# Optimization experiments

Measured on AMD Instinct MI355X. Metric: run time of the kernel, lower is better.

The kernel has to match this reference:

```python
import jax, jax.numpy as jnp
import numpy as np
from jax import lax

T = 64      # timesteps == number of stacked LSTM layers (per source)
B = 128     # lstm_batchsize (hardcoded)
H = 64      # BasicLSTMCell(64)


def _cell(x_in, c, h, W, b):
    # TF BasicLSTMCell, forget_bias=0.0, gate order: i, j, f, o
    z = jnp.concatenate([x_in, h], axis=-1) @ W + b          # [B, 4H]
    i, j, f, o = jnp.split(z, 4, axis=-1)
    c2 = c * jax.nn.sigmoid(f) + jax.nn.sigmoid(i) * jnp.tanh(j)
    h2 = jnp.tanh(c2) * jax.nn.sigmoid(o)
    return c2, h2


def setup_inputs() -> dict:
    key = jax.random.key(0)
    ks = jax.random.split(key, 8)
    s = 0.1
    x = jax.random.normal(ks[0], (B, T, 1), dtype=jnp.float32)
    labels = jax.random.normal(ks[1], (B, T, 1), dtype=jnp.float32)
    # layer 0: input dim 1; layers 1..T-1: input dim H
    W0 = jax.random.normal(ks[2], (1 + H, 4 * H), dtype=jnp.float32) * s
    b0 = jnp.zeros((4 * H,), dtype=jnp.float32)
    Wl = jax.random.normal(ks[3], (T - 1, H + H, 4 * H), dtype=jnp.float32) * s
    bl = jnp.zeros((T - 1, 4 * H), dtype=jnp.float32)
    # time_distributed fully_connected(1, relu): separate weights per timestep
    Wd = jax.random.normal(ks[4], (T, H, 1), dtype=jnp.float32) * s
    bd = jnp.zeros((T, 1), dtype=jnp.float32)
    return {"x": x, "labels": labels, "W0": W0, "b0": b0,
            "Wl": Wl, "bl": bl, "Wd": Wd, "bd": bd}


def reference(x, labels, W0, b0, Wl, bl, Wd, bd):
    def step(carry, x_t):
        cs, hs = carry                      # each [T, B, H]
        c0, h0 = _cell(x_t, cs[0], hs[0], W0, b0)

        def layer_step(h_in, lp):
            c, h_prev, W, b = lp
            c2, h2 = _cell(h_in, c, h_prev, W, b)
            return h2, (c2, h2)

        h_top, (cs_r, hs_r) = lax.scan(layer_step, h0, (cs[1:], hs[1:], Wl, bl))
        new_cs = jnp.concatenate([c0[None], cs_r], axis=0)
        new_hs = jnp.concatenate([h0[None], hs_r], axis=0)
        return (new_cs, new_hs), h_top

    init = (jnp.zeros((T, B, H), x.dtype), jnp.zeros((T, B, H), x.dtype))
    xs = jnp.transpose(x, (1, 0, 2))        # [T, B, 1]
    _, outs = lax.scan(step, init, xs)      # outs: [T, B, H]
    outs = jnp.transpose(outs, (1, 0, 2))   # [B, T, H]

    # per-timestep dense + relu
    pred = jax.nn.relu(jnp.einsum('bth,tho->bto', outs, Wd) + bd[None])  # [B, T, 1]
    loss = jnp.mean(jnp.square(labels - pred))
    return pred, loss
```

## Files before the change

### kernel.cpp

```cpp
#include <hip/hip_runtime.h>
#include <hip/hip_bf16.h>
#include <hip/hip_fp8.h>

#define TT 64
#define LL 64
#define BB 128
#define HH 64
#define NP 32
#define SL 8
#define RR 16

typedef short v8s __attribute__((ext_vector_type(8)));
typedef float v4f __attribute__((ext_vector_type(4)));


__device__ __forceinline__ float sigm(float z)   {
    return __builtin_amdgcn_rcpf(1.f + __expf(-z));
}
__device__ __forceinline__ float tanh_f(float z) {
    return fmaf(-2.f, __builtin_amdgcn_rcpf(1.f + __expf(2.f * z)), 1.f);
}
__device__ __forceinline__ unsigned long long gload64(const unsigned long long* p) {
    return __hip_atomic_load(p, __ATOMIC_RELAXED, __HIP_MEMORY_SCOPE_AGENT);
}
__device__ __forceinline__ void gstore64(unsigned long long* p, unsigned long long v) {
    __hip_atomic_store(p, v, __ATOMIC_RELAXED, __HIP_MEMORY_SCOPE_AGENT);
}
__device__ __forceinline__ int fload(const int* p) {
    return __hip_atomic_load(p, __ATOMIC_RELAXED, __HIP_MEMORY_SCOPE_AGENT);
}
__device__ __forceinline__ void fstore(int* p, int v) {
    __hip_atomic_store(p, v, __ATOMIC_RELAXED, __HIP_MEMORY_SCOPE_AGENT);
}
__device__ __forceinline__ unsigned short f2bf(float f) {
    unsigned u = __float_as_uint(f);
    return (unsigned short)((u + 0x8000u) >> 16);
}

__global__ __launch_bounds__(512, 2) void lstm_pipeline(
    const float* __restrict__ x,
    const float* __restrict__ W0,
    const float* __restrict__ b0,
    const float* __restrict__ Wl,
    const float* __restrict__ bl,
    int* __restrict__ prog,
    unsigned long long* __restrict__ hglob,
    float* __restrict__ htop)
{
    const int p   = blockIdx.x >> 3;
    const int s   = blockIdx.x & 7;
    const int tid = threadIdx.x;
    const int wv  = tid >> 6;
    const int la  = wv >> 2;
    const int w   = wv & 3;
    const int ln  = tid & 63;
    const int lr  = ln & 15;
    const int qd  = ln >> 4;
    const int l   = 2 * p + la;

    __shared__ unsigned short hA[2][RR * 72];
    __shared__ unsigned short hB[2][RR * 72];
    __shared__ float xbuf[RR * 65];

    if (blockIdx.x == 0 && tid < 2) fstore(&prog[300 + tid], 0);

    for (int i = tid; i < RR * 72; i += 512) {
        hA[0][i] = 0; hA[1][i] = 0; hB[0][i] = 0; hB[1][i] = 0;
    }
    if (p == 0) {
        for (int i = tid; i < RR * 64; i += 512)
            xbuf[(i >> 6) * 65 + (i & 63)] =
                x[(size_t)(s * RR + (i >> 6)) * TT + (i & 63)];
    }

    v8s bfr[16];
#pragma unroll
    for (int f = 0; f < 16; ++f) {
        const int ga = f >> 2, kf = f & 3;
        const int gc = ga * 64 + w * 16 + lr;
        v8s tmp;
#pragma unroll
        for (int j = 0; j < 8; ++j) {
            const int k = kf * 32 + qd * 8 + j;
            float v;
            if (l > 0)       v = Wl[((size_t)(l - 1) * 128 + k) * 256 + gc];
            else if (k == 0) v = W0[gc];
            else if (k < 64) v = 0.f;
            else             v = W0[(size_t)(k - 63) * 256 + gc];
            tmp[j] = (short)f2bf(v);
        }
        bfr[f] = tmp;
    }

    const float* bs = l ? (bl + (l - 1) * 256) : b0;
    float bias[4];
#pragma unroll
    for (int ga = 0; ga < 4; ++ga) bias[ga] = bs[ga * 64 + w * 16 + lr];

    float cst[4];
#pragma unroll
    for (int i = 0; i < 4; ++i) cst[i] = 0.f;

    __syncthreads();

    for (int t = 0; t < TT; ++t) {
        const int cur = t & 1;

        if (la == 0) {
            unsigned int belowW[4];
            if (p > 0) {
                const unsigned long long* rp =
                    hglob + ((((size_t)(t & 15) * NP + (p - 1)) * SL + s) * RR + lr) * 16;
                for (;;) {
                    unsigned long long v0 = gload64(rp + qd * 2);
                    unsigned long long v1 = gload64(rp + qd * 2 + 1);
                    unsigned long long v2 = gload64(rp + 8 + qd * 2);
                    unsigned long long v3 = gload64(rp + 8 + qd * 2 + 1);
                    unsigned int ok =
                        (unsigned int)((unsigned int)(v0 >> 32) == (unsigned int)t) &
                        (unsigned int)((unsigned int)(v1 >> 32) == (unsigned int)t) &
                        (unsigned int)((unsigned int)(v2 >> 32) == (unsigned int)t) &
                        (unsigned int)((unsigned int)(v3 >> 32) == (unsigned int)t);
                    if (ok) {
                        belowW[0] = (unsigned int)v0; belowW[1] = (unsigned int)v1;
                        belowW[2] = (unsigned int)v2; belowW[3] = (unsigned int)v3;
                        break;
                    }
                }
                if (tid == 0) fstore(&prog[s * NP + p], t + 1);
            }

            v4f acc[4];
#pragma unroll
            for (int i = 0; i < 4; ++i) acc[i] = (v4f){0.f, 0.f, 0.f, 0.f};

            const int row = lr * 72;
            v8s a2 = *(const v8s*)&hA[cur ^ 1][row + qd * 8];
            v8s a3 = *(const v8s*)&hA[cur ^ 1][row + 32 + qd * 8];
            v8s a0, a1;
            if (p > 0) {
#pragma unroll
                for (int wi = 0; wi < 2; ++wi)
#pragma unroll
                    for (int bi = 0; bi < 4; ++bi) {
                        __hip_fp8_e4m3 f8;
                        f8.__x = (belowW[wi] >> (8 * bi)) & 0xff;
                        a0[wi * 4 + bi] = (short)f2bf((float)f8);
                        f8.__x = (belowW[2 + wi] >> (8 * bi)) & 0xff;
                        a1[wi * 4 + bi] = (short)f2bf((float)f8);
                    }
            } else {
                a0 = (v8s){0, 0, 0, 0, 0, 0, 0, 0};
                a1 = (v8s){0, 0, 0, 0, 0, 0, 0, 0};
                if (qd == 0) a0[0] = (short)f2bf(xbuf[lr * 65 + t]);
            }
#pragma unroll
            for (int ga = 0; ga < 4; ++ga) {
                v4f c = acc[ga];
                c = __builtin_amdgcn_mfma_f32_16x16x32_bf16(a2, bfr[ga * 4 + 2], c, 0, 0, 0);
                c = __builtin_amdgcn_mfma_f32_16x16x32_bf16(a3, bfr[ga * 4 + 3], c, 0, 0, 0);
                c = __builtin_amdgcn_mfma_f32_16x16x32_bf16(a0, bfr[ga * 4 + 0], c, 0, 0, 0);
                c = __builtin_amdgcn_mfma_f32_16x16x32_bf16(a1, bfr[ga * 4 + 1], c, 0, 0, 0);
                acc[ga] = c;
            }
#pragma unroll
            for (int r = 0; r < 4; ++r) {
                float zi = acc[0][r] + bias[0];
                float zj = acc[1][r] + bias[1];
                float zf = acc[2][r] + bias[2];
                float zo = acc[3][r] + bias[3];
                float c2 = cst[r] * sigm(zf) + sigm(zi) * tanh_f(zj);
                cst[r] = c2;
                float h2 = tanh_f(c2) * sigm(zo);
                hA[cur][(qd * 4 + r) * 72 + w * 16 + lr] = f2bf(h2);
            }
        }

        __syncthreads();

        if (la == 1) {
            int gate = 0;
            if (p < NP - 1 && t >= 15)
                gate = fload(&prog[s * NP + (p + 1)]);

            v4f acc[4];
#pragma unroll
            for (int i = 0; i < 4; ++i) acc[i] = (v4f){0.f, 0.f, 0.f, 0.f};

            const int row = lr * 72;
            v8s a2 = *(const v8s*)&hB[cur ^ 1][row + qd * 8];
            v8s a3 = *(const v8s*)&hB[cur ^ 1][row + 32 + qd * 8];
            v8s a0 = *(const v8s*)&hA[cur][row + qd * 8];
            v8s a1 = *(const v8s*)&hA[cur][row + 32 + qd * 8];
#pragma unroll
            for (int ga = 0; ga < 4; ++ga) {
                v4f c = acc[ga];
                c = __builtin_amdgcn_mfma_f32_16x16x32_bf16(a2, bfr[ga * 4 + 2], c, 0, 0, 0);
                c = __builtin_amdgcn_mfma_f32_16x16x32_bf16(a3, bfr[ga * 4 + 3], c, 0, 0, 0);
                c = __builtin_amdgcn_mfma_f32_16x16x32_bf16(a0, bfr[ga * 4 + 0], c, 0, 0, 0);
                c = __builtin_amdgcn_mfma_f32_16x16x32_bf16(a1, bfr[ga * 4 + 1], c, 0, 0, 0);
                acc[ga] = c;
            }
            if (p < NP - 1 && t >= 15 && gate < t - 14)
                while (fload(&prog[s * NP + (p + 1)]) < t - 14) {}

            unsigned long long* dst =
                hglob + ((((size_t)(t & 15) * NP + p) * SL + s) * RR) * 16;
#pragma unroll
            for (int r = 0; r < 4; ++r) {
                float zi = acc[0][r] + bias[0];
                float zj = acc[1][r] + bias[1];
                float zf = acc[2][r] + bias[2];
                float zo = acc[3][r] + bias[3];
                float c2 = cst[r] * sigm(zf) + sigm(zi) * tanh_f(zj);
                cst[r] = c2;
                float h2 = tanh_f(c2) * sigm(zo);
                const int b = qd * 4 + r;
                const int u = w * 16 + lr;
                hB[cur][b * 72 + u] = f2bf(h2);
                if (p < NP - 1) {
                    __hip_fp8_e4m3 f8(h2);
                    unsigned int pk = ((unsigned int)f8.__x) << (8 * (lr & 3));
                    pk |= __shfl_xor(pk, 1);
                    pk |= __shfl_xor(pk, 2);
                    if ((lr & 3) == 0)
                        gstore64(dst + (size_t)b * 16 + w * 4 + (lr >> 2),
                                 (unsigned long long)pk |
                                 ((unsigned long long)(unsigned int)t << 32));
                } else {
                    htop[((size_t)t * HH + u) * BB + s * RR + b] = h2;
                }
            }
        }
    }
}

__global__ __launch_bounds__(128, 1) void epilogue(
    const float* __restrict__ htop, const float* __restrict__ Wd,
    const float* __restrict__ bd, const float* __restrict__ labels,
    float* __restrict__ out, int* __restrict__ prog)
{
    int t = blockIdx.x, b = threadIdx.x;
    float s = 0.f;
#pragma unroll 4
    for (int h = 0; h < HH; ++h)
        s = fmaf(htop[(size_t)t * HH * BB + h * BB + b], Wd[t * HH + h], s);
    s += bd[t];
    s = fmaxf(s, 0.f);
    out[b * TT + t] = s;
    float d = labels[b * TT + t] - s;
    float e = d * d;
#pragma unroll
    for (int off = 32; off > 0; off >>= 1) e += __shfl_down(e, off, 64);
    __shared__ float ws2[2];
    if ((b & 63) == 0) ws2[b >> 6] = e;
    __syncthreads();
    if (b == 0) {
        float* loss = (float*)&prog[300];
        atomicAdd(loss, ws2[0] + ws2[1]);
        __builtin_amdgcn_s_waitcnt(0);
        int done = __hip_atomic_fetch_add(&prog[301], 1, __ATOMIC_ACQ_REL,
                                          __HIP_MEMORY_SCOPE_AGENT);
        if (done == 63) {
            float tot = __hip_atomic_load(loss, __ATOMIC_RELAXED,
                                          __HIP_MEMORY_SCOPE_AGENT);
            out[BB * TT] = tot * (1.f / (BB * TT));
        }
    }
}

extern "C" void kernel_launch(void* const* d_in, const int* in_sizes, int n_in,
                              void* d_out, int out_size, void* d_ws, size_t ws_size,
                              hipStream_t stream) {
    const float* x      = (const float*)d_in[0];
    const float* labels = (const float*)d_in[1];
    const float* W0     = (const float*)d_in[2];
    const float* b0     = (const float*)d_in[3];
    const float* Wl     = (const float*)d_in[4];
    const float* bl     = (const float*)d_in[5];
    const float* Wd     = (const float*)d_in[6];
    const float* bd     = (const float*)d_in[7];
    float* out = (float*)d_out;

    char* base = (char*)d_ws;
    int*                prog  = (int*)base;
    unsigned long long* hglob = (unsigned long long*)(base + 16384);
    float*              htop  = (float*)(base + 16384 + 8388608);

    lstm_pipeline<<<NP * SL, 512, 0, stream>>>(x, W0, b0, Wl, bl, prog, hglob, htop);
    epilogue<<<64, 128, 0, stream>>>(htop, Wd, bd, labels, out, prog);
}
```

Baseline: 577.4 us.

## Pack four layers per block with in-block wavefront skew over timesteps

Each block now handles four consecutive layers instead of two. Pairs of waves own one layer and split the 64 hidden units in half, and the layers run as a diagonal wavefront inside the block, with layer k lagging k steps and one barrier per superstep. This halves the number of inter-block global handoffs (fp8 hglob and flag polling) and the grid size, cutting cross-block sync latency along the layer chain. In exchange each wave holds twice the weight fragments (32 v8s), adds GG-1 pipeline fill steps, and puts more serial work in each block.

```diff
diff --git a/kernel.cpp b/kernel.cpp
--- a/kernel.cpp
+++ b/kernel.cpp
@@ -6,9 +6,11 @@
 #define LL 64
 #define BB 128
 #define HH 64
-#define NP 32
+#define GG 4
+#define NG 16
 #define SL 8
 #define RR 16
+#define SB (TT + GG - 1)
 
 typedef short v8s __attribute__((ext_vector_type(8)));
 typedef float v4f __attribute__((ext_vector_type(4)));
@@ -47,70 +49,81 @@
     unsigned long long* __restrict__ hglob,
     float* __restrict__ htop)
 {
-    const int p   = blockIdx.x >> 3;
+    const int g   = blockIdx.x >> 3;
     const int s   = blockIdx.x & 7;
     const int tid = threadIdx.x;
     const int wv  = tid >> 6;
-    const int la  = wv >> 2;
-    const int w   = wv & 3;
+    const int k   = wv >> 1;
+    const int nh  = wv & 1;
     const int ln  = tid & 63;
     const int lr  = ln & 15;
     const int qd  = ln >> 4;
-    const int l   = 2 * p + la;
-
-    __shared__ unsigned short hA[2][RR * 72];
-    __shared__ unsigned short hB[2][RR * 72];
+    const int l   = GG * g + k;
+
+    __shared__ unsigned short hL[GG][2][RR * 72];
     __shared__ float xbuf[RR * 65];
 
     if (blockIdx.x == 0 && tid < 2) fstore(&prog[300 + tid], 0);
 
-    for (int i = tid; i < RR * 72; i += 512) {
-        hA[0][i] = 0; hA[1][i] = 0; hB[0][i] = 0; hB[1][i] = 0;
-    }
-    if (p == 0) {
+    for (int i = tid; i < GG * 2 * RR * 72; i += 512)
+        ((unsigned short*)hL)[i] = 0;
+    if (g == 0) {
         for (int i = tid; i < RR * 64; i += 512)
             xbuf[(i >> 6) * 65 + (i & 63)] =
                 x[(size_t)(s * RR + (i >> 6)) * TT + (i & 63)];
     }
 
-    v8s bfr[16];
-#pragma unroll
-    for (int f = 0; f < 16; ++f) {
-        const int ga = f >> 2, kf = f & 3;
-        const int gc = ga * 64 + w * 16 + lr;
+    v8s bfr[32];
+#pragma unroll
+    for (int f = 0; f < 32; ++f) {
+        const int kf = f & 3, tn = f >> 2;
+        const int ga = tn & 3, ut = tn >> 2;
+        const int gc = ga * 64 + nh * 32 + ut * 16 + lr;
         v8s tmp;
 #pragma unroll
         for (int j = 0; j < 8; ++j) {
-            const int k = kf * 32 + qd * 8 + j;
+            const int kk = kf * 32 + qd * 8 + j;
             float v;
-            if (l > 0)       v = Wl[((size_t)(l - 1) * 128 + k) * 256 + gc];
-            else if (k == 0) v = W0[gc];
-            else if (k < 64) v = 0.f;
-            else             v = W0[(size_t)(k - 63) * 256 + gc];
+            if (l > 0)        v = Wl[((size_t)(l - 1) * 128 + kk) * 256 + gc];
+            else if (kk == 0) v = W0[gc];
+            else if (kk < 64) v = 0.f;
+            else              v = W0[(size_t)(kk - 63) * 256 + gc];
             tmp[j] = (short)f2bf(v);
         }
         bfr[f] = tmp;
     }
 
     const float* bs = l ? (bl + (l - 1) * 256) : b0;
-    float bias[4];
-#pragma unroll
-    for (int ga = 0; ga < 4; ++ga) bias[ga] = bs[ga * 64 + w * 16 + lr];
-
-    float cst[4];
-#pragma unroll
-    for (int i = 0; i < 4; ++i) cst[i] = 0.f;
+    float bias[8];
+#pragma unroll
+    for (int i = 0; i < 8; ++i) {
+        const int ut = i >> 2, ga = i & 3;
+        bias[i] = bs[ga * 64 + nh * 32 + ut * 16 + lr];
+    }
+
+    float cst[8];
+#pragma unroll
+    for (int i = 0; i < 8; ++i) cst[i] = 0.f;
 
     __syncthreads();
 
-    for (int t = 0; t < TT; ++t) {
-        const int cur = t & 1;
-
-        if (la == 0) {
-            unsigned int belowW[4];
-            if (p > 0) {
+    for (int sb = 0; sb < SB; ++sb) {
+        const int t = sb - k;
+        const bool active = (t >= 0) && (t < TT);
+        const int rd = (sb - 1) & 1, wr = sb & 1;
+
+        if (active) {
+            const int row = lr * 72;
+            v8s a2 = *(const v8s*)&hL[k][rd][row + qd * 8];
+            v8s a3 = *(const v8s*)&hL[k][rd][row + 32 + qd * 8];
+            v8s a0, a1;
+            if (k > 0) {
+                a0 = *(const v8s*)&hL[k - 1][rd][row + qd * 8];
+                a1 = *(const v8s*)&hL[k - 1][rd][row + 32 + qd * 8];
+            } else if (g > 0) {
                 const unsigned long long* rp =
-                    hglob + ((((size_t)(t & 15) * NP + (p - 1)) * SL + s) * RR + lr) * 16;
+                    hglob + ((((size_t)(t & 15) * NG + (g - 1)) * SL + s) * RR + lr) * 16;
+                unsigned int bw0, bw1, bw2, bw3;
                 for (;;) {
                     unsigned long long v0 = gload64(rp + qd * 2);
                     unsigned long long v1 = gload64(rp + qd * 2 + 1);
@@ -122,31 +135,21 @@
                         (unsigned int)((unsigned int)(v2 >> 32) == (unsigned int)t) &
                         (unsigned int)((unsigned int)(v3 >> 32) == (unsigned int)t);
                     if (ok) {
-                        belowW[0] = (unsigned int)v0; belowW[1] = (unsigned int)v1;
-                        belowW[2] = (unsigned int)v2; belowW[3] = (unsigned int)v3;
+                        bw0 = (unsigned int)v0; bw1 = (unsigned int)v1;
+                        bw2 = (unsigned int)v2; bw3 = (unsigned int)v3;
                         break;
                     }
                 }
-                if (tid == 0) fstore(&prog[s * NP + p], t + 1);
-            }
-
-            v4f acc[4];
-#pragma unroll
-            for (int i = 0; i < 4; ++i) acc[i] = (v4f){0.f, 0.f, 0.f, 0.f};
-
-            const int row = lr * 72;
-            v8s a2 = *(const v8s*)&hA[cur ^ 1][row + qd * 8];
-            v8s a3 = *(const v8s*)&hA[cur ^ 1][row + 32 + qd * 8];
-            v8s a0, a1;
-            if (p > 0) {
+                if (nh == 0 && ln == 0) fstore(&prog[s * NG + g], t + 1);
+                unsigned int ws4[4] = {bw0, bw1, bw2, bw3};
 #pragma unroll
                 for (int wi = 0; wi < 2; ++wi)
 #pragma unroll
                     for (int bi = 0; bi < 4; ++bi) {
                         __hip_fp8_e4m3 f8;
-                        f8.__x = (belowW[wi] >> (8 * bi)) & 0xff;
+                        f8.__x = (ws4[wi] >> (8 * bi)) & 0xff;
                         a0[wi * 4 + bi] = (short)f2bf((float)f8);
-                        f8.__x = (belowW[2 + wi] >> (8 * bi)) & 0xff;
+                        f8.__x = (ws4[2 + wi] >> (8 * bi)) & 0xff;
                         a1[wi * 4 + bi] = (short)f2bf((float)f8);
                     }
             } else {
@@ -154,84 +157,57 @@
                 a1 = (v8s){0, 0, 0, 0, 0, 0, 0, 0};
                 if (qd == 0) a0[0] = (short)f2bf(xbuf[lr * 65 + t]);
             }
-#pragma unroll
-            for (int ga = 0; ga < 4; ++ga) {
-                v4f c = acc[ga];
-                c = __builtin_amdgcn_mfma_f32_16x16x32_bf16(a2, bfr[ga * 4 + 2], c, 0, 0, 0);
-                c = __builtin_amdgcn_mfma_f32_16x16x32_bf16(a3, bfr[ga * 4 + 3], c, 0, 0, 0);
-                c = __builtin_amdgcn_mfma_f32_16x16x32_bf16(a0, bfr[ga * 4 + 0], c, 0, 0, 0);
-                c = __builtin_amdgcn_mfma_f32_16x16x32_bf16(a1, bfr[ga * 4 + 1], c, 0, 0, 0);
-                acc[ga] = c;
+
+            v4f acc[8];
+#pragma unroll
+            for (int i = 0; i < 8; ++i) acc[i] = (v4f){0.f, 0.f, 0.f, 0.f};
+#pragma unroll
+            for (int tn = 0; tn < 8; ++tn) {
+                v4f c = acc[tn];
+                c = __builtin_amdgcn_mfma_f32_16x16x32_bf16(a2, bfr[tn * 4 + 2], c, 0, 0, 0);
+                c = __builtin_amdgcn_mfma_f32_16x16x32_bf16(a3, bfr[tn * 4 + 3], c, 0, 0, 0);
+                c = __builtin_amdgcn_mfma_f32_16x16x32_bf16(a0, bfr[tn * 4 + 0], c, 0, 0, 0);
+                c = __builtin_amdgcn_mfma_f32_16x16x32_bf16(a1, bfr[tn * 4 + 1], c, 0, 0, 0);
+                acc[tn] = c;
             }
-#pragma unroll
-            for (int r = 0; r < 4; ++r) {
-                float zi = acc[0][r] + bias[0];
-                float zj = acc[1][r] + bias[1];
-                float zf = acc[2][r] + bias[2];
-                float zo = acc[3][r] + bias[3];
-                float c2 = cst[r] * sigm(zf) + sigm(zi) * tanh_f(zj);
-                cst[r] = c2;
-                float h2 = tanh_f(c2) * sigm(zo);
-                hA[cur][(qd * 4 + r) * 72 + w * 16 + lr] = f2bf(h2);
-            }
-        }
-
-        __syncthreads();
-
-        if (la == 1) {
-            int gate = 0;
-            if (p < NP - 1 && t >= 15)
-                gate = fload(&prog[s * NP + (p + 1)]);
-
-            v4f acc[4];
-#pragma unroll
-            for (int i = 0; i < 4; ++i) acc[i] = (v4f){0.f, 0.f, 0.f, 0.f};
-
-            const int row = lr * 72;
-            v8s a2 = *(const v8s*)&hB[cur ^ 1][row + qd * 8];
-            v8s a3 = *(const v8s*)&hB[cur ^ 1][row + 32 + qd * 8];
-            v8s a0 = *(const v8s*)&hA[cur][row + qd * 8];
-            v8s a1 = *(const v8s*)&hA[cur][row + 32 + qd * 8];
-#pragma unroll
-            for (int ga = 0; ga < 4; ++ga) {
-                v4f c = acc[ga];
-                c = __builtin_amdgcn_mfma_f32_16x16x32_bf16(a2, bfr[ga * 4 + 2], c, 0, 0, 0);
-                c = __builtin_amdgcn_mfma_f32_16x16x32_bf16(a3, bfr[ga * 4 + 3], c, 0, 0, 0);
-                c = __builtin_amdgcn_mfma_f32_16x16x32_bf16(a0, bfr[ga * 4 + 0], c, 0, 0, 0);
-                c = __builtin_amdgcn_mfma_f32_16x16x32_bf16(a1, bfr[ga * 4 + 1], c, 0, 0, 0);
-                acc[ga] = c;
-            }
-            if (p < NP - 1 && t >= 15 && gate < t - 14)
-                while (fload(&prog[s * NP + (p + 1)]) < t - 14) {}
+
+            if (k == 3 && g < NG - 1 && t >= 14)
+                while (fload(&prog[s * NG + (g + 1)]) < t - 14) {}
 
             unsigned long long* dst =
-                hglob + ((((size_t)(t & 15) * NP + p) * SL + s) * RR) * 16;
-#pragma unroll
-            for (int r = 0; r < 4; ++r) {
-                float zi = acc[0][r] + bias[0];
-                float zj = acc[1][r] + bias[1];
-                float zf = acc[2][r] + bias[2];
-                float zo = acc[3][r] + bias[3];
-                float c2 = cst[r] * sigm(zf) + sigm(zi) * tanh_f(zj);
-                cst[r] = c2;
-                float h2 = tanh_f(c2) * sigm(zo);
-                const int b = qd * 4 + r;
-                const int u = w * 16 + lr;
-                hB[cur][b * 72 + u] = f2bf(h2);
-                if (p < NP - 1) {
-                    __hip_fp8_e4m3 f8(h2);
-                    unsigned int pk = ((unsigned int)f8.__x) << (8 * (lr & 3));
-                    pk |= __shfl_xor(pk, 1);
-                    pk |= __shfl_xor(pk, 2);
-                    if ((lr & 3) == 0)
-                        gstore64(dst + (size_t)b * 16 + w * 4 + (lr >> 2),
-                                 (unsigned long long)pk |
-                                 ((unsigned long long)(unsigned int)t << 32));
-                } else {
-                    htop[((size_t)t * HH + u) * BB + s * RR + b] = h2;
+                hglob + ((((size_t)(t & 15) * NG + g) * SL + s) * RR) * 16;
+#pragma unroll
+            for (int ut = 0; ut < 2; ++ut) {
+                const int u = nh * 32 + ut * 16 + lr;
+#pragma unroll
+                for (int r = 0; r < 4; ++r) {
+                    float zi = acc[ut * 4 + 0][r] + bias[ut * 4 + 0];
+                    float zj = acc[ut * 4 + 1][r] + bias[ut * 4 + 1];
+                    float zf = acc[ut * 4 + 2][r] + bias[ut * 4 + 2];
+                    float zo = acc[ut * 4 + 3][r] + bias[ut * 4 + 3];
+                    float c2 = cst[ut * 4 + r] * sigm(zf) + sigm(zi) * tanh_f(zj);
+                    cst[ut * 4 + r] = c2;
+                    float h2 = tanh_f(c2) * sigm(zo);
+                    const int b = qd * 4 + r;
+                    hL[k][wr][b * 72 + u] = f2bf(h2);
+                    if (k == 3) {
+                        if (g < NG - 1) {
+                            __hip_fp8_e4m3 f8(h2);
+                            unsigned int pk = ((unsigned int)f8.__x) << (8 * (lr & 3));
+                            pk |= __shfl_xor(pk, 1);
+                            pk |= __shfl_xor(pk, 2);
+                            if ((lr & 3) == 0)
+                                gstore64(dst + (size_t)b * 16 + nh * 8 + ut * 4 + (lr >> 2),
+                                         (unsigned long long)pk |
+                                         ((unsigned long long)(unsigned int)t << 32));
+                        } else {
+                            htop[((size_t)t * HH + u) * BB + s * RR + b] = h2;
+                        }
+                    }
                 }
             }
         }
+        __syncthreads();
     }
 }
 
@@ -285,8 +261,8 @@
     char* base = (char*)d_ws;
     int*                prog  = (int*)base;
     unsigned long long* hglob = (unsigned long long*)(base + 16384);
-    float*              htop  = (float*)(base + 16384 + 8388608);
-
-    lstm_pipeline<<<NP * SL, 512, 0, stream>>>(x, W0, b0, Wl, bl, prog, hglob, htop);
+    float*              htop  = (float*)(base + 16384 + 4194304);
+
+    lstm_pipeline<<<NG * SL, 512, 0, stream>>>(x, W0, b0, Wl, bl, prog, hglob, htop);
     epilogue<<<64, 128, 0, stream>>>(htop, Wd, bd, labels, out, prog);
 }
```

New measurement: 510.4 us. 1.13x faster.
